# Kernel tuning notes

Measured on AMD Instinct MI355X. Metric: run time of the kernel, lower is better.

The kernel has to match this reference:

```python
import jax, jax.numpy as jnp
import numpy as np

B, D, O, E, H, K = 4096, 1024, 1024, 8, 4096, 2


def setup_inputs() -> dict:
    key = jax.random.key(0)
    ks = jax.random.split(key, 5)
    scale_g = 1.0 / np.sqrt(D)
    scale_1 = 1.0 / np.sqrt(D)
    scale_2 = 1.0 / np.sqrt(H)
    return {
        "x": jax.random.normal(ks[0], (B, D), jnp.float32),
        "gate_w": jax.random.normal(ks[1], (D, E), jnp.float32) * scale_g,
        "gate_b": jnp.zeros((E,), jnp.float32),
        "w1": jax.random.normal(ks[2], (E, D, H), jnp.float32) * scale_1,
        "b1": jnp.zeros((E, H), jnp.float32),
        "w2": jax.random.normal(ks[3], (E, H, O), jnp.float32) * scale_2,
        "b2": jnp.zeros((E, O), jnp.float32),
    }


def reference(x, gate_w, gate_b, w1, b1, w2, b2):
    # Router: top-k logits, softmax over the k selected logits only
    logits = x @ gate_w + gate_b                      # [B, E]
    top_vals, top_idx = jax.lax.top_k(logits, K)      # [B, K]
    routing_w = jax.nn.softmax(top_vals, axis=-1)     # [B, K]

    # Dense all-expert MLP (grouped GEMM), then gather the k selected outputs
    h = jax.nn.relu(jnp.einsum("bd,edh->beh", x, w1) + b1)  # [B, E, H]
    y = jnp.einsum("beh,eho->beo", h, w2) + b2              # [B, E, O]
    sel = jnp.take_along_axis(y, top_idx[:, :, None], axis=1)  # [B, K, O]
    return jnp.sum(routing_w[:, :, None] * sel, axis=1)        # [B, O]
```

## Files before the change

### kernel.cpp

```cpp
#include <hip/hip_runtime.h>
#include <stdint.h>

typedef short bf16x8 __attribute__((ext_vector_type(8)));
typedef float f32x4  __attribute__((ext_vector_type(4)));

constexpr int BT = 4096;
constexpr int DD = 1024;
constexpr int OO = 1024;
constexpr int EE = 8;
constexpr int HH = 4096;
constexpr int SLOTS = 2 * BT;

__device__ __forceinline__ unsigned short f2bf(float f) {
  unsigned u = __float_as_uint(f);
  u += 0x7fffu + ((u >> 16) & 1u);
  return (unsigned short)(u >> 16);
}

__device__ __forceinline__ void glds16(const unsigned short* g, unsigned short* l) {
  __builtin_amdgcn_global_load_lds(
      (const __attribute__((address_space(1))) void*)g,
      (__attribute__((address_space(3))) void*)l, 16, 0, 0);
}

__global__ __launch_bounds__(256) void router_k(const float* __restrict__ x,
                                                const float* __restrict__ gw,
                                                const float* __restrict__ gb,
                                                unsigned short* __restrict__ xb,
                                                int* __restrict__ cnt,
                                                int* __restrict__ list,
                                                float* __restrict__ rw) {
  int wave = threadIdx.x >> 6, lane = threadIdx.x & 63;
  int b = blockIdx.x * 4 + wave;
  const float* xrow = x + (size_t)b * DD;
  float acc[8];
#pragma unroll
  for (int e = 0; e < 8; ++e) acc[e] = 0.f;
#pragma unroll
  for (int i = 0; i < 4; ++i) {
    int d0 = i * 256 + lane * 4;
    float4 v = *(const float4*)&xrow[d0];
    unsigned lo = (unsigned)f2bf(v.x) | ((unsigned)f2bf(v.y) << 16);
    unsigned hi = (unsigned)f2bf(v.z) | ((unsigned)f2bf(v.w) << 16);
    *(uint2*)&xb[(size_t)b * DD + d0] = make_uint2(lo, hi);
    const float* g0 = &gw[(size_t)d0 * 8];
    float fv[4] = {v.x, v.y, v.z, v.w};
#pragma unroll
    for (int q = 0; q < 4; ++q) {
      float4 ga = *(const float4*)&g0[q * 8];
      float4 gc = *(const float4*)&g0[q * 8 + 4];
      acc[0] += fv[q] * ga.x; acc[1] += fv[q] * ga.y;
      acc[2] += fv[q] * ga.z; acc[3] += fv[q] * ga.w;
      acc[4] += fv[q] * gc.x; acc[5] += fv[q] * gc.y;
      acc[6] += fv[q] * gc.z; acc[7] += fv[q] * gc.w;
    }
  }
#pragma unroll
  for (int off = 32; off > 0; off >>= 1) {
#pragma unroll
    for (int e = 0; e < 8; ++e) acc[e] += __shfl_down(acc[e], off);
  }
  if (lane == 0) {
    float v[8];
#pragma unroll
    for (int e = 0; e < 8; ++e) v[e] = acc[e] + gb[e];
    int i0 = 0;
#pragma unroll
    for (int e = 1; e < 8; ++e) if (v[e] > v[i0]) i0 = e;
    int i1 = (i0 == 0) ? 1 : 0;
#pragma unroll
    for (int e = 0; e < 8; ++e) if (e != i0 && v[e] > v[i1]) i1 = e;
    float e1 = __expf(v[i1] - v[i0]);
    float inv = 1.0f / (1.0f + e1);
    int p0 = atomicAdd(&cnt[i0], 1);
    list[i0 * BT + p0] = 2 * b;     rw[2 * b]     = inv;
    int p1 = atomicAdd(&cnt[i1], 1);
    list[i1 * BT + p1] = 2 * b + 1; rw[2 * b + 1] = e1 * inv;
  }
}

__global__ void tilemap_k(const int* __restrict__ cnt, int* __restrict__ tmap,
                          int* __restrict__ ntiles) {
  if (threadIdx.x == 0 && blockIdx.x == 0) {
    int t = 0, basewalk = 0;
    for (int e = 0; e < EE; ++e) {
      int c = cnt[e];
      for (int m0 = 0; m0 < c; m0 += 128) {
        tmap[4 * t] = e; tmap[4 * t + 1] = m0; tmap[4 * t + 2] = basewalk + m0; ++t;
      }
      basewalk += c;
    }
    *ntiles = t;
  }
}

__global__ __launch_bounds__(256) void cvt_t_k(const float* __restrict__ src,
                                               unsigned short* __restrict__ dst,
                                               int R, int C) {
  __shared__ unsigned short tile[64][66];
  int e = blockIdx.z;
  const float* s = src + (size_t)e * R * C;
  unsigned short* d = dst + (size_t)e * R * C;
  int r0 = blockIdx.x << 6, c0 = blockIdx.y << 6;
  int t = threadIdx.x;
#pragma unroll
  for (int p = 0; p < 4; ++p) {
    int ch = p * 256 + t;
    int rr = ch >> 4, cc = (ch & 15) << 2;
    float4 v = *(const float4*)&s[(size_t)(r0 + rr) * C + c0 + cc];
    unsigned lo = (unsigned)f2bf(v.x) | ((unsigned)f2bf(v.y) << 16);
    unsigned hi = (unsigned)f2bf(v.z) | ((unsigned)f2bf(v.w) << 16);
    *(uint2*)&tile[rr][cc] = make_uint2(lo, hi);
  }
  __syncthreads();
#pragma unroll
  for (int p = 0; p < 4; ++p) {
    int ch = p * 256 + t;
    int cc = ch >> 4, rr = (ch & 15) << 2;
    unsigned short v0 = tile[rr + 0][cc];
    unsigned short v1 = tile[rr + 1][cc];
    unsigned short v2 = tile[rr + 2][cc];
    unsigned short v3 = tile[rr + 3][cc];
    unsigned lo = (unsigned)v0 | ((unsigned)v1 << 16);
    unsigned hi = (unsigned)v2 | ((unsigned)v3 << 16);
    *(uint2*)&d[(size_t)(c0 + cc) * R + r0 + rr] = make_uint2(lo, hi);
  }
}

__global__ __launch_bounds__(256, 4) void gemm1_k(const unsigned short* __restrict__ xb,
                                                  const unsigned short* __restrict__ w1t,
                                                  const float* __restrict__ b1,
                                                  const int* __restrict__ cnt,
                                                  const int* __restrict__ list,
                                                  const int* __restrict__ tmap,
                                                  const int* __restrict__ ntiles,
                                                  unsigned short* __restrict__ hc) {
  int ti = blockIdx.y;
  if (ti >= *ntiles) return;
  int e = tmap[4 * ti], m0 = tmap[4 * ti + 1], base = tmap[4 * ti + 2];
  int cnt_e = cnt[e];
  int n0 = blockIdx.x * 128;

  __shared__ int slotbuf[128];
  __shared__ __align__(16) unsigned short Ash[128 * 64];
  __shared__ __align__(16) unsigned short Bsh[128 * 64];

  int t = threadIdx.x;
  if (t < 128) {
    int r = m0 + t;
    slotbuf[t] = list[e * BT + (r < cnt_e ? r : 0)];
  }
  __syncthreads();

  int w = t >> 6, l = t & 63;
  int lm = l & 15, lq = l >> 4;
  int wm = (w & 1) * 64, wn = (w >> 1) * 64;

  const unsigned short* Bsrc = w1t + (size_t)e * HH * DD + (size_t)n0 * DD;

  const unsigned short* aS[4];
  const unsigned short* bS[4];
  unsigned short* aL[4];
  unsigned short* bL[4];
#pragma unroll
  for (int j = 0; j < 4; ++j) {
    int idx = 4 * w + j;
    int row = idx * 8 + (l >> 3);
    int koff = (l & 7) * 8;
    int tok = slotbuf[row] >> 1;
    aS[j] = xb + (size_t)tok * DD + koff;
    bS[j] = Bsrc + (size_t)row * DD + koff;
    aL[j] = &Ash[idx * 512];
    bL[j] = &Bsh[idx * 512];
  }

  f32x4 acc[4][4];
#pragma unroll
  for (int mi = 0; mi < 4; ++mi)
#pragma unroll
    for (int ni = 0; ni < 4; ++ni) acc[mi][ni] = f32x4{0.f, 0.f, 0.f, 0.f};

  for (int k0 = 0; k0 < DD; k0 += 64) {
#pragma unroll
    for (int j = 0; j < 4; ++j) glds16(aS[j] + k0, aL[j]);
#pragma unroll
    for (int j = 0; j < 4; ++j) glds16(bS[j] + k0, bL[j]);
    __syncthreads();
#pragma unroll
    for (int ks = 0; ks < 2; ++ks) {
      bf16x8 af[4], bfr[4];
      int kb = ks * 32 + lq * 8;
#pragma unroll
      for (int mi = 0; mi < 4; ++mi)
        af[mi] = *(const bf16x8*)&Ash[(wm + mi * 16 + lm) * 64 + kb];
#pragma unroll
      for (int ni = 0; ni < 4; ++ni)
        bfr[ni] = *(const bf16x8*)&Bsh[(wn + ni * 16 + lm) * 64 + kb];
#pragma unroll
      for (int mi = 0; mi < 4; ++mi)
#pragma unroll
        for (int ni = 0; ni < 4; ++ni)
          acc[mi][ni] = __builtin_amdgcn_mfma_f32_16x16x32_bf16(af[mi], bfr[ni], acc[mi][ni], 0, 0, 0);
    }
    __syncthreads();
  }

#pragma unroll
  for (int ni = 0; ni < 4; ++ni) {
    int ncol = n0 + wn + ni * 16 + lm;
    float bias = b1[e * HH + ncol];
#pragma unroll
    for (int mi = 0; mi < 4; ++mi) {
      int mbase = wm + mi * 16 + lq * 4;
#pragma unroll
      for (int r = 0; r < 4; ++r) {
        int mrow = mbase + r;
        if (m0 + mrow < cnt_e) {
          float v = fmaxf(acc[mi][ni][r] + bias, 0.0f);
          hc[(size_t)(base + mrow) * HH + ncol] = f2bf(v);
        }
      }
    }
  }
}

__global__ __launch_bounds__(256, 4) void gemm2_k(const unsigned short* __restrict__ hc,
                                                  const unsigned short* __restrict__ w2t,
                                                  const float* __restrict__ b2,
                                                  const int* __restrict__ cnt,
                                                  const int* __restrict__ list,
                                                  const int* __restrict__ tmap,
                                                  const int* __restrict__ ntiles,
                                                  const float* __restrict__ rw,
                                                  float* __restrict__ ybuf,
                                                  float* __restrict__ out) {
  int ti = blockIdx.y;
  if (ti >= *ntiles) return;
  int e = tmap[4 * ti], m0 = tmap[4 * ti + 1], base = tmap[4 * ti + 2];
  int cnt_e = cnt[e];
  int n0 = blockIdx.x * 128;
  int ksl = HH / gridDim.z;
  int kb0 = blockIdx.z * ksl;

  __shared__ int slotbuf[128];
  __shared__ float rwbuf[128];
  __shared__ __align__(16) unsigned short Ash[128 * 64];
  __shared__ __align__(16) unsigned short Bsh[128 * 64];

  int t = threadIdx.x;
  if (t < 128) {
    int r = m0 + t;
    int s_ = list[e * BT + (r < cnt_e ? r : 0)];
    slotbuf[t] = s_;
    rwbuf[t] = rw[s_];
  }
  __syncthreads();

  int w = t >> 6, l = t & 63;
  int lm = l & 15, lq = l >> 4;
  int wm = (w & 1) * 64, wn = (w >> 1) * 64;

  const unsigned short* Bsrc = w2t + (size_t)e * OO * HH + (size_t)n0 * HH;

  const unsigned short* aS[4];
  const unsigned short* bS[4];
  unsigned short* aL[4];
  unsigned short* bL[4];
#pragma unroll
  for (int j = 0; j < 4; ++j) {
    int idx = 4 * w + j;
    int row = idx * 8 + (l >> 3);
    int koff = (l & 7) * 8;
    aS[j] = hc + (size_t)(base + row) * HH + kb0 + koff;
    bS[j] = Bsrc + (size_t)row * HH + kb0 + koff;
    aL[j] = &Ash[idx * 512];
    bL[j] = &Bsh[idx * 512];
  }

  f32x4 acc[4][4];
#pragma unroll
  for (int mi = 0; mi < 4; ++mi)
#pragma unroll
    for (int ni = 0; ni < 4; ++ni) acc[mi][ni] = f32x4{0.f, 0.f, 0.f, 0.f};

  for (int k0 = 0; k0 < ksl; k0 += 64) {
#pragma unroll
    for (int j = 0; j < 4; ++j) glds16(aS[j] + k0, aL[j]);
#pragma unroll
    for (int j = 0; j < 4; ++j) glds16(bS[j] + k0, bL[j]);
    __syncthreads();
#pragma unroll
    for (int ks = 0; ks < 2; ++ks) {
      bf16x8 af[4], bfr[4];
      int kb = ks * 32 + lq * 8;
#pragma unroll
      for (int mi = 0; mi < 4; ++mi)
        af[mi] = *(const bf16x8*)&Ash[(wm + mi * 16 + lm) * 64 + kb];
#pragma unroll
      for (int ni = 0; ni < 4; ++ni)
        bfr[ni] = *(const bf16x8*)&Bsh[(wn + ni * 16 + lm) * 64 + kb];
#pragma unroll
      for (int mi = 0; mi < 4; ++mi)
#pragma unroll
        for (int ni = 0; ni < 4; ++ni)
          acc[mi][ni] = __builtin_amdgcn_mfma_f32_16x16x32_bf16(af[mi], bfr[ni], acc[mi][ni], 0, 0, 0);
    }
    __syncthreads();
  }

  bool addbias = (blockIdx.z == 0);
  size_t ybase = (size_t)blockIdx.z * SLOTS;
#pragma unroll
  for (int ni = 0; ni < 4; ++ni) {
    int ncol = n0 + wn + ni * 16 + lm;
    float bias = addbias ? b2[e * OO + ncol] : 0.0f;
#pragma unroll
    for (int mi = 0; mi < 4; ++mi) {
      int mbase = wm + mi * 16 + lq * 4;
#pragma unroll
      for (int r = 0; r < 4; ++r) {
        int mrow = mbase + r;
        if (m0 + mrow < cnt_e) {
          float v = (acc[mi][ni][r] + bias) * rwbuf[mrow];
          int slot = slotbuf[mrow];
          if (ybuf) ybuf[(ybase + slot) * OO + ncol] = v;
          else      atomicAdd(&out[(size_t)(slot >> 1) * OO + ncol], v);
        }
      }
    }
  }
}

__global__ __launch_bounds__(256) void combine_k(const float* __restrict__ y,
                                                 float* __restrict__ out, int nz) {
  int i = blockIdx.x * 256 + threadIdx.x;
  int b = i >> 8, c = i & 255;
  f32x4 acc = {0.f, 0.f, 0.f, 0.f};
  for (int z = 0; z < nz; ++z) {
#pragma unroll
    for (int k = 0; k < 2; ++k) {
      const float4 v = *(const float4*)&y[((size_t)z * SLOTS + 2 * b + k) * OO + c * 4];
      acc[0] += v.x; acc[1] += v.y; acc[2] += v.z; acc[3] += v.w;
    }
  }
  *(f32x4*)&out[(size_t)b * OO + c * 4] = acc;
}

extern "C" void kernel_launch(void* const* d_in, const int* in_sizes, int n_in,
                              void* d_out, int out_size, void* d_ws, size_t ws_size,
                              hipStream_t stream) {
  const float* x  = (const float*)d_in[0];
  const float* gw = (const float*)d_in[1];
  const float* gb = (const float*)d_in[2];
  const float* w1 = (const float*)d_in[3];
  const float* b1 = (const float*)d_in[4];
  const float* w2 = (const float*)d_in[5];
  const float* b2 = (const float*)d_in[6];
  float* out = (float*)d_out;
  char* ws = (char*)d_ws;

  int*            cnt    = (int*)(ws);
  int*            ntiles = (int*)(ws + 64);
  int*            tmap   = (int*)(ws + 128);
  float*          rw     = (float*)(ws + 4096);
  int*            list   = (int*)(ws + (64u << 10));
  unsigned short* xb     = (unsigned short*)(ws + (1u  << 20));
  unsigned short* wt     = (unsigned short*)(ws + (9u  << 20));
  unsigned short* hc     = (unsigned short*)(ws + (73u << 20));
  float*          ybuf   = (float*)(ws + (138u << 20));

  size_t need_min = (138u << 20);
  if (ws_size < need_min) return;
  int zsplit;
  float* ypass;
  if (ws_size >= (138u << 20) + (size_t)2 * SLOTS * OO * 4) { zsplit = 2; ypass = ybuf; }
  else if (ws_size >= (138u << 20) + (size_t)SLOTS * OO * 4) { zsplit = 1; ypass = ybuf; }
  else { zsplit = 2; ypass = nullptr; }

  hipMemsetAsync(cnt, 0, 64, stream);
  if (!ypass) hipMemsetAsync(out, 0, (size_t)BT * OO * sizeof(float), stream);

  router_k<<<BT / 4, 256, 0, stream>>>(x, gw, gb, xb, cnt, list, rw);
  tilemap_k<<<1, 64, 0, stream>>>(cnt, tmap, ntiles);
  cvt_t_k<<<dim3(DD / 64, HH / 64, EE), 256, 0, stream>>>(w1, wt, DD, HH);
  gemm1_k<<<dim3(HH / 128, 72), 256, 0, stream>>>(xb, wt, b1, cnt, list, tmap, ntiles, hc);
  cvt_t_k<<<dim3(HH / 64, OO / 64, EE), 256, 0, stream>>>(w2, wt, HH, OO);
  gemm2_k<<<dim3(OO / 128, 72, zsplit), 256, 0, stream>>>(hc, wt, b2, cnt, list, tmap, ntiles, rw, ypass, out);
  if (ypass)
    combine_k<<<BT * OO / 1024, 256, 0, stream>>>(ybuf, out, zsplit);
}
```

Measured before the change: 718.9 us.

## Enlarge gemm2 M-tile to 256 rows and stage gemm1 epilogue through LDS

gemm2 now uses 512-thread blocks covering 256 token rows per expert tile, driven by a second tile map, so each loaded W2 tile is reused across twice as many rows and fewer blocks are launched. gemm1's epilogue writes results into a padded shared buffer and then stores 16-byte coalesced rows to hc, replacing the scattered 2-byte stores. In exchange, gemm2 uses more LDS and more threads per block, which may lower occupancy, and ragged experts waste more of each larger tile. The unseen gemm2 epilogue has to handle 256 rows for results to stay correct.

Result: no change. 726.3 us (+1.0%).

```diff
diff --git a/kernel.cpp b/kernel.cpp
--- a/kernel.cpp
+++ b/kernel.cpp
@@ -79,18 +79,23 @@
   }
 }
 
-__global__ void tilemap_k(const int* __restrict__ cnt, int* __restrict__ tmap,
-                          int* __restrict__ ntiles) {
+__global__ void tilemap_k(const int* __restrict__ cnt,
+                          int* __restrict__ tA, int* __restrict__ ntA,
+                          int* __restrict__ tB, int* __restrict__ ntB) {
   if (threadIdx.x == 0 && blockIdx.x == 0) {
-    int t = 0, basewalk = 0;
+    int a = 0, b = 0, basewalk = 0;
     for (int e = 0; e < EE; ++e) {
       int c = cnt[e];
       for (int m0 = 0; m0 < c; m0 += 128) {
-        tmap[4 * t] = e; tmap[4 * t + 1] = m0; tmap[4 * t + 2] = basewalk + m0; ++t;
+        tA[4 * a] = e; tA[4 * a + 1] = m0; tA[4 * a + 2] = basewalk + m0; ++a;
+      }
+      for (int m0 = 0; m0 < c; m0 += 256) {
+        tB[4 * b] = e; tB[4 * b + 1] = m0; tB[4 * b + 2] = basewalk + m0; ++b;
       }
       basewalk += c;
     }
-    *ntiles = t;
+    *ntA = a;
+    *ntB = b;
   }
 }
 
@@ -142,8 +147,9 @@
   int n0 = blockIdx.x * 128;
 
   __shared__ int slotbuf[128];
-  __shared__ __align__(16) unsigned short Ash[128 * 64];
-  __shared__ __align__(16) unsigned short Bsh[128 * 64];
+  __shared__ __align__(16) unsigned short smem[128 * 136];
+  unsigned short* Ash = smem;
+  unsigned short* Bsh = smem + 128 * 64;
 
   int t = threadIdx.x;
   if (t < 128) {
@@ -207,24 +213,29 @@
 
 #pragma unroll
   for (int ni = 0; ni < 4; ++ni) {
-    int ncol = n0 + wn + ni * 16 + lm;
-    float bias = b1[e * HH + ncol];
+    int col = wn + ni * 16 + lm;
+    float bias = b1[e * HH + n0 + col];
 #pragma unroll
     for (int mi = 0; mi < 4; ++mi) {
-      int mbase = wm + mi * 16 + lq * 4;
-#pragma unroll
-      for (int r = 0; r < 4; ++r) {
-        int mrow = mbase + r;
-        if (m0 + mrow < cnt_e) {
-          float v = fmaxf(acc[mi][ni][r] + bias, 0.0f);
-          hc[(size_t)(base + mrow) * HH + ncol] = f2bf(v);
-        }
-      }
-    }
-  }
-}
-
-__global__ __launch_bounds__(256, 4) void gemm2_k(const unsigned short* __restrict__ hc,
+      int rbase = wm + mi * 16 + lq * 4;
+#pragma unroll
+      for (int r = 0; r < 4; ++r)
+        smem[(rbase + r) * 136 + col] = f2bf(fmaxf(acc[mi][ni][r] + bias, 0.0f));
+    }
+  }
+  __syncthreads();
+  int rr = t >> 4, cl = (t & 15) * 8;
+#pragma unroll
+  for (int p = 0; p < 8; ++p) {
+    int row = p * 16 + rr;
+    if (m0 + row < cnt_e) {
+      bf16x8 v = *(const bf16x8*)&smem[row * 136 + cl];
+      *(bf16x8*)&hc[(size_t)(base + row) * HH + n0 + cl] = v;
+    }
+  }
+}
+
+__global__ __launch_bounds__(512, 4) void gemm2_k(const unsigned short* __restrict__ hc,
                                                   const unsigned short* __restrict__ w2t,
                                                   const float* __restrict__ b2,
                                                   const int* __restrict__ cnt,
@@ -242,13 +253,13 @@
   int ksl = HH / gridDim.z;
   int kb0 = blockIdx.z * ksl;
 
-  __shared__ int slotbuf[128];
-  __shared__ float rwbuf[128];
-  __shared__ __align__(16) unsigned short Ash[128 * 64];
+  __shared__ int slotbuf[256];
+  __shared__ float rwbuf[256];
+  __shared__ __align__(16) unsigned short Ash[256 * 64];
   __shared__ __align__(16) unsigned short Bsh[128 * 64];
 
   int t = threadIdx.x;
-  if (t < 128) {
+  if (t < 256) {
     int r = m0 + t;
     int s_ = list[e * BT + (r < cnt_e ? r : 0)];
     slotbuf[t] = s_;
@@ -258,22 +269,28 @@
 
   int w = t >> 6, l = t & 63;
   int lm = l & 15, lq = l >> 4;
-  int wm = (w & 1) * 64, wn = (w >> 1) * 64;
+  int wm = (w & 3) * 64, wn = (w >> 2) * 64;
 
   const unsigned short* Bsrc = w2t + (size_t)e * OO * HH + (size_t)n0 * HH;
 
   const unsigned short* aS[4];
-  const unsigned short* bS[4];
+  const unsigned short* bS[2];
   unsigned short* aL[4];
-  unsigned short* bL[4];
+  unsigned short* bL[2];
 #pragma unroll
   for (int j = 0; j < 4; ++j) {
     int idx = 4 * w + j;
     int row = idx * 8 + (l >> 3);
     int koff = (l & 7) * 8;
     aS[j] = hc + (size_t)(base + row) * HH + kb0 + koff;
+    aL[j] = &Ash[idx * 512];
+  }
+#pragma unroll
+  for (int j = 0; j < 2; ++j) {
+    int idx = 2 * w + j;
+    int row = idx * 8 + (l >> 3);
+    int koff = (l & 7) * 8;
     bS[j] = Bsrc + (size_t)row * HH + kb0 + koff;
-    aL[j] = &Ash[idx * 512];
     bL[j] = &Bsh[idx * 512];
   }
 
@@ -287,7 +304,7 @@
 #pragma unroll
     for (int j = 0; j < 4; ++j) glds16(aS[j] + k0, aL[j]);
 #pragma unroll
-    for (int j = 0; j < 4; ++j) glds16(bS[j] + k0, bL[j]);
+    for (int j = 0; j < 2; ++j) glds16(bS[j] + k0, bL[j]);
     __syncthreads();
 #pragma unroll
     for (int ks = 0; ks < 2; ++ks) {
@@ -360,32 +377,34 @@
   char* ws = (char*)d_ws;
 
   int*            cnt    = (int*)(ws);
-  int*            ntiles = (int*)(ws + 64);
-  int*            tmap   = (int*)(ws + 128);
+  int*            ntA    = (int*)(ws + 64);
+  int*            ntB    = (int*)(ws + 68);
+  int*            tmapA  = (int*)(ws + 128);
+  int*            tmapB  = (int*)(ws + 2048);
   float*          rw     = (float*)(ws + 4096);
   int*            list   = (int*)(ws + (64u << 10));
   unsigned short* xb     = (unsigned short*)(ws + (1u  << 20));
   unsigned short* wt     = (unsigned short*)(ws + (9u  << 20));
   unsigned short* hc     = (unsigned short*)(ws + (73u << 20));
-  float*          ybuf   = (float*)(ws + (138u << 20));
-
-  size_t need_min = (138u << 20);
+  float*          ybuf   = (float*)(ws + (140u << 20));
+
+  size_t need_min = (140u << 20);
   if (ws_size < need_min) return;
   int zsplit;
   float* ypass;
-  if (ws_size >= (138u << 20) + (size_t)2 * SLOTS * OO * 4) { zsplit = 2; ypass = ybuf; }
-  else if (ws_size >= (138u << 20) + (size_t)SLOTS * OO * 4) { zsplit = 1; ypass = ybuf; }
+  if (ws_size >= (140u << 20) + (size_t)2 * SLOTS * OO * 4) { zsplit = 2; ypass = ybuf; }
+  else if (ws_size >= (140u << 20) + (size_t)SLOTS * OO * 4) { zsplit = 1; ypass = ybuf; }
   else { zsplit = 2; ypass = nullptr; }
 
   hipMemsetAsync(cnt, 0, 64, stream);
   if (!ypass) hipMemsetAsync(out, 0, (size_t)BT * OO * sizeof(float), stream);
 
   router_k<<<BT / 4, 256, 0, stream>>>(x, gw, gb, xb, cnt, list, rw);
-  tilemap_k<<<1, 64, 0, stream>>>(cnt, tmap, ntiles);
+  tilemap_k<<<1, 64, 0, stream>>>(cnt, tmapA, ntA, tmapB, ntB);
   cvt_t_k<<<dim3(DD / 64, HH / 64, EE), 256, 0, stream>>>(w1, wt, DD, HH);
-  gemm1_k<<<dim3(HH / 128, 72), 256, 0, stream>>>(xb, wt, b1, cnt, list, tmap, ntiles, hc);
+  gemm1_k<<<dim3(HH / 128, 72), 256, 0, stream>>>(xb, wt, b1, cnt, list, tmapA, ntA, hc);
   cvt_t_k<<<dim3(HH / 64, OO / 64, EE), 256, 0, stream>>>(w2, wt, HH, OO);
-  gemm2_k<<<dim3(OO / 128, 72, zsplit), 256, 0, stream>>>(hc, wt, b2, cnt, list, tmap, ntiles, rw, ypass, out);
+  gemm2_k<<<dim3(OO / 128, 40, zsplit), 512, 0, stream>>>(hc, wt, b2, cnt, list, tmapB, ntB, rw, ypass, out);
   if (ypass)
     combine_k<<<BT * OO / 1024, 256, 0, stream>>>(ybuf, out, zsplit);
 }
```
